# Kernel tuning notes

Measured on AMD Instinct MI355X. Metric: run time of the kernel, lower is better.

## Reference

```python
import jax, jax.numpy as jnp
import numpy as np

EPS = 1e-8  # torch F.cosine_similarity norm clamp


def setup_inputs() -> dict:
    key = jax.random.key(0)
    k1, k2, k3, k4 = jax.random.split(key, 4)
    B, N, M, D, T = 8, 4096, 2048, 512, 2
    return {
        "features": jax.random.normal(k1, (B, N, D), dtype=jnp.float32),
        "text": jax.random.normal(k2, (T, M, D), dtype=jnp.float32),
        "W": jax.random.normal(k3, (D, D), dtype=jnp.float32) * 0.02,
        "b": jax.random.normal(k4, (D,), dtype=jnp.float32) * 0.02,
    }


def reference(features, text, W, b):
    # features: [B, N, D] (output of the extractor), text: [T, M, D]
    B, N, D = features.shape
    f1 = jnp.einsum("bnd,de->bne", features, W) + b  # linear_layer(features)
    t1 = text[1]  # [M, D]; expanded across batch (row 1 per original code)

    # cosine similarity over last dim without materializing [B, N, M, D]
    fn = f1 / jnp.maximum(jnp.linalg.norm(f1, axis=-1, keepdims=True), EPS)
    tn = t1 / jnp.maximum(jnp.linalg.norm(t1, axis=-1, keepdims=True), EPS)
    sim = jnp.einsum("bnd,md->bnm", fn, tn)  # [B, N, M]

    e = jnp.exp(sim)
    w = e / jnp.sum(e, axis=1, keepdims=True)  # normalize over N (dim=1)

    # features_t [B,D,N] @ w [B,N,M] -> [B,D,M] -> transpose -> [B,M,D]
    fm = jnp.einsum("bnd,bnm->bmd", features, w)

    t1b = jnp.broadcast_to(t1[None, :, :], (B,) + t1.shape)  # [B, M, D]
    combine_feature = jnp.concatenate([fm, t1b], axis=2)  # [B, M, 2D]
    return combine_feature
```

## Files before the change

kernel.cpp:

```cpp
#include <hip/hip_runtime.h>

#define B_SZ 8
#define N_SZ 4096
#define M_SZ 2048
#define D_SZ 512

typedef __attribute__((ext_vector_type(8))) short bf16x8;
typedef __attribute__((ext_vector_type(4))) float f32x4;
typedef __attribute__((address_space(1))) const void* gptr1;
typedef __attribute__((address_space(3))) void* lptr3;

__device__ __forceinline__ unsigned short f2bf(float x) {
    unsigned int u = __builtin_bit_cast(unsigned int, x);
    u += 0x7fffu + ((u >> 16) & 1u);
    return (unsigned short)(u >> 16);
}

__device__ __forceinline__ void bt_mainloop(
    const unsigned short* __restrict__ A, const unsigned short* __restrict__ Bt,
    int lda, int ldb, int rowBase, int colBase, int K,
    unsigned short* As, unsigned short* Bs, f32x4 acc[4][4])
{
    const int tid  = threadIdx.x;
    const int lane = tid & 63;
    const int w    = tid >> 6;
    const int wr   = (w >> 1) * 64;
    const int wc   = (w & 1) * 64;
    const int lr   = lane & 15;
    const int kq   = lane >> 4;

    const int srow0 = w * 16 + (lane >> 2);
    const int skk   = (lane & 3) * 8;

    for (int k0 = 0; k0 < K; k0 += 32) {
#pragma unroll
        for (int j = 0; j < 2; ++j) {
            const unsigned short* ga = A  + (size_t)(rowBase + srow0 + j * 64) * lda + (k0 + skk);
            const unsigned short* gb = Bt + (size_t)(colBase + srow0 + j * 64) * ldb + (k0 + skk);
            __builtin_amdgcn_global_load_lds((gptr1)ga, (lptr3)(As + (j * 4 + w) * 512), 16, 0, 0);
            __builtin_amdgcn_global_load_lds((gptr1)gb, (lptr3)(Bs + (j * 4 + w) * 512), 16, 0, 0);
        }
        asm volatile("s_waitcnt vmcnt(0)" ::: "memory");
        __syncthreads();

        bf16x8 af[4], bq[4];
#pragma unroll
        for (int i = 0; i < 4; ++i) {
            af[i] = *(const bf16x8*)(As + (wr + i * 16 + lr) * 32 + kq * 8);
            bq[i] = *(const bf16x8*)(Bs + (wc + i * 16 + lr) * 32 + kq * 8);
        }
#pragma unroll
        for (int mi = 0; mi < 4; ++mi)
#pragma unroll
            for (int ni = 0; ni < 4; ++ni)
                acc[mi][ni] = __builtin_amdgcn_mfma_f32_16x16x32_bf16(af[mi], bq[ni], acc[mi][ni], 0, 0, 0);
        __syncthreads();
    }
}

#define GEMM_PROLOGUE() \
    __shared__ unsigned short As[128 * 32]; \
    __shared__ unsigned short Bs[128 * 32]; \
    f32x4 acc[4][4]; \
    _Pragma("unroll") for (int i = 0; i < 4; ++i) \
        _Pragma("unroll") for (int j = 0; j < 4; ++j) \
            acc[i][j] = (f32x4){0.f, 0.f, 0.f, 0.f}; \
    const int tid = threadIdx.x; const int lane = tid & 63; const int w = tid >> 6; \
    const int wr = (w >> 1) * 64, wc = (w & 1) * 64, lr = lane & 15, kq = lane >> 4; \
    (void)tid;

__global__ __launch_bounds__(256) void prep_tn_k(
    const float* __restrict__ text, unsigned short* __restrict__ tn,
    float* __restrict__ out, float* __restrict__ L)
{
    const int m = blockIdx.x;
    const int t = threadIdx.x;
    const float* t1 = text + (size_t)M_SZ * D_SZ;
    float2 v = ((const float2*)(t1 + (size_t)m * D_SZ))[t];
    float s = v.x * v.x + v.y * v.y;
#pragma unroll
    for (int off = 32; off > 0; off >>= 1) s += __shfl_down(s, off);
    __shared__ float partial[4];
    if ((t & 63) == 0) partial[t >> 6] = s;
    __syncthreads();
    float norm = sqrtf(partial[0] + partial[1] + partial[2] + partial[3]);
    norm = fmaxf(norm, 1e-8f);
    const float inv = 1.f / norm;
    ushort2 pk; pk.x = f2bf(v.x * inv); pk.y = f2bf(v.y * inv);
    ((ushort2*)(tn + (size_t)m * D_SZ))[t] = pk;
#pragma unroll
    for (int b = 0; b < B_SZ; ++b)
        ((float2*)(out + ((size_t)(b * M_SZ + m)) * (2 * D_SZ) + D_SZ))[t] = v;
    if (m < 64) L[m * 256 + t] = 0.f;
}

__global__ __launch_bounds__(256) void prep_w_k(
    const float* __restrict__ W, unsigned short* __restrict__ Wt)
{
    const int dt = blockIdx.x, et = blockIdx.y;
    const int t = threadIdx.x;
    __shared__ unsigned short tile[64][72];
    const int rr = t >> 4;
    const int cc = (t & 15) * 4;
#pragma unroll
    for (int p = 0; p < 4; ++p) {
        const int d = p * 16 + rr;
        const float4 v = *(const float4*)(W + (size_t)(dt * 64 + d) * D_SZ + et * 64 + cc);
        tile[d][cc] = f2bf(v.x); tile[d][cc + 1] = f2bf(v.y);
        tile[d][cc + 2] = f2bf(v.z); tile[d][cc + 3] = f2bf(v.w);
    }
    __syncthreads();
#pragma unroll
    for (int p = 0; p < 4; ++p) {
        const int e = p * 16 + rr;
        ushort4 pk;
        pk.x = tile[cc][e]; pk.y = tile[cc + 1][e]; pk.z = tile[cc + 2][e]; pk.w = tile[cc + 3][e];
        *(ushort4*)(Wt + (size_t)(et * 64 + e) * D_SZ + dt * 64 + cc) = pk;
    }
}

__global__ __launch_bounds__(256) void convert_feat_k(
    const float* __restrict__ feat, unsigned short* __restrict__ V,
    unsigned short* __restrict__ Vt)
{
    const int nt = blockIdx.x, dt = blockIdx.y, b = blockIdx.z;
    const int t = threadIdx.x;
    __shared__ unsigned short tile[64][72];
    const int rr = t >> 4;
    const int cc = (t & 15) * 4;
#pragma unroll
    for (int p = 0; p < 4; ++p) {
        const int r = p * 16 + rr;
        const size_t grow = (size_t)(b * N_SZ + nt * 64 + r);
        const float4 v = *(const float4*)(feat + grow * D_SZ + dt * 64 + cc);
        ushort4 pk; pk.x = f2bf(v.x); pk.y = f2bf(v.y); pk.z = f2bf(v.z); pk.w = f2bf(v.w);
        *(ushort4*)(V + grow * D_SZ + dt * 64 + cc) = pk;
        tile[r][cc] = pk.x; tile[r][cc + 1] = pk.y; tile[r][cc + 2] = pk.z; tile[r][cc + 3] = pk.w;
    }
    __syncthreads();
#pragma unroll
    for (int p = 0; p < 4; ++p) {
        const int d = p * 16 + rr;
        ushort4 pk;
        pk.x = tile[cc][d]; pk.y = tile[cc + 1][d]; pk.z = tile[cc + 2][d]; pk.w = tile[cc + 3][d];
        *(ushort4*)(Vt + ((size_t)(b * D_SZ + dt * 64 + d)) * N_SZ + nt * 64 + cc) = pk;
    }
}

__global__ __launch_bounds__(256) void gemm1_k(
    const unsigned short* __restrict__ V, const unsigned short* __restrict__ Wt,
    const float* __restrict__ bias, float* __restrict__ f1)
{
    GEMM_PROLOGUE();
    const int rowBase = blockIdx.x * 128;
    const int colBase = blockIdx.y * 128;
    bt_mainloop(V, Wt, D_SZ, D_SZ, rowBase, colBase, D_SZ, As, Bs, acc);
#pragma unroll
    for (int mi = 0; mi < 4; ++mi) {
        const int r0 = rowBase + wr + mi * 16 + kq * 4;
#pragma unroll
        for (int ni = 0; ni < 4; ++ni) {
            const int c = colBase + wc + ni * 16 + lr;
            const float bv = bias[c];
#pragma unroll
            for (int r = 0; r < 4; ++r)
                f1[(size_t)(r0 + r) * D_SZ + c] = acc[mi][ni][r] + bv;
        }
    }
}

__global__ __launch_bounds__(128) void normalize_k(
    const float* __restrict__ f1, unsigned short* __restrict__ fn)
{
    const int row = blockIdx.x;
    const int t = threadIdx.x;
    const float4 v = ((const float4*)(f1 + (size_t)row * D_SZ))[t];
    float s = v.x * v.x + v.y * v.y + v.z * v.z + v.w * v.w;
#pragma unroll
    for (int off = 32; off > 0; off >>= 1) s += __shfl_down(s, off);
    __shared__ float partial[2];
    if ((t & 63) == 0) partial[t >> 6] = s;
    __syncthreads();
    float norm = sqrtf(partial[0] + partial[1]);
    norm = fmaxf(norm, 1e-8f);
    const float inv = 1.f / norm;
    ushort4 pk;
    pk.x = f2bf(v.x * inv); pk.y = f2bf(v.y * inv);
    pk.z = f2bf(v.z * inv); pk.w = f2bf(v.w * inv);
    ((ushort4*)(fn + (size_t)row * D_SZ))[t] = pk;
}

__global__ __launch_bounds__(256) void gemm2_k(
    const unsigned short* __restrict__ fn, const unsigned short* __restrict__ tn,
    unsigned short* __restrict__ E, float* __restrict__ L)
{
    GEMM_PROLOGUE();
    const int rowBase = blockIdx.x * 128;
    const int colBase = blockIdx.y * 128;
    bt_mainloop(fn, tn, D_SZ, D_SZ, rowBase, colBase, D_SZ, As, Bs, acc);

    const int b  = rowBase >> 12;
    const int nb = rowBase & 4095;
    unsigned short* Eb = E + (size_t)b * M_SZ * N_SZ;
#pragma unroll
    for (int ni = 0; ni < 4; ++ni) {
        const int m = colBase + wc + ni * 16 + lr;
        float p = 0.f;
#pragma unroll
        for (int mi = 0; mi < 4; ++mi) {
            const int n0 = nb + wr + mi * 16 + kq * 4;
            const float e0 = __expf(acc[mi][ni][0]);
            const float e1 = __expf(acc[mi][ni][1]);
            const float e2 = __expf(acc[mi][ni][2]);
            const float e3 = __expf(acc[mi][ni][3]);
            ushort4 pk; pk.x = f2bf(e0); pk.y = f2bf(e1); pk.z = f2bf(e2); pk.w = f2bf(e3);
            *(ushort4*)(Eb + (size_t)m * N_SZ + n0) = pk;
            p += (e0 + e1) + (e2 + e3);
        }
        p += __shfl_down(p, 16);
        p += __shfl_down(p, 32);
        if (lane < 16) atomicAdd(&L[b * M_SZ + m], p);
    }
}

__global__ __launch_bounds__(256) void gemm3_k(
    const unsigned short* __restrict__ E, const unsigned short* __restrict__ Vt,
    const float* __restrict__ L, float* __restrict__ out)
{
    GEMM_PROLOGUE();
    const int b = blockIdx.z;
    const int rowBase = blockIdx.x * 128;
    const int colBase = blockIdx.y * 128;
    const unsigned short* Ab = E + (size_t)b * M_SZ * N_SZ;
    const unsigned short* Bb = Vt + (size_t)b * D_SZ * N_SZ;
    bt_mainloop(Ab, Bb, N_SZ, N_SZ, rowBase, colBase, N_SZ, As, Bs, acc);

#pragma unroll
    for (int mi = 0; mi < 4; ++mi) {
        const int r0 = rowBase + wr + mi * 16 + kq * 4;
        float invl[4];
#pragma unroll
        for (int r = 0; r < 4; ++r) invl[r] = 1.f / L[b * M_SZ + r0 + r];
#pragma unroll
        for (int ni = 0; ni < 4; ++ni) {
            const int d = colBase + wc + ni * 16 + lr;
#pragma unroll
            for (int r = 0; r < 4; ++r)
                out[((size_t)(b * M_SZ + r0 + r)) * (2 * D_SZ) + d] = acc[mi][ni][r] * invl[r];
        }
    }
}

extern "C" void kernel_launch(void* const* d_in, const int* in_sizes, int n_in,
                              void* d_out, int out_size, void* d_ws, size_t ws_size,
                              hipStream_t stream) {
    const float* features = (const float*)d_in[0];
    const float* text     = (const float*)d_in[1];
    const float* W        = (const float*)d_in[2];
    const float* bias     = (const float*)d_in[3];
    float* out = (float*)d_out;
    char* ws = (char*)d_ws;

    unsigned short* fn = (unsigned short*)(ws + 0);
    unsigned short* tn = (unsigned short*)(ws + 33554432);
    unsigned short* Wt = (unsigned short*)(ws + 35651584);
    unsigned short* V  = (unsigned short*)(ws + 36175872);
    unsigned short* Vt = (unsigned short*)(ws + 69730304);
    float*          L  = (float*)(ws + 103284736);
    float*          f1 = (float*)(ws + 103350272);
    unsigned short* E  = (unsigned short*)(ws + 103350272);

    hipLaunchKernelGGL(prep_tn_k, dim3(M_SZ), dim3(256), 0, stream, text, tn, out, L);
    hipLaunchKernelGGL(prep_w_k, dim3(8, 8), dim3(256), 0, stream, W, Wt);
    hipLaunchKernelGGL(convert_feat_k, dim3(64, 8, 8), dim3(256), 0, stream, features, V, Vt);
    hipLaunchKernelGGL(gemm1_k, dim3(256, 4), dim3(256), 0, stream, V, Wt, bias, f1);
    hipLaunchKernelGGL(normalize_k, dim3(32768), dim3(128), 0, stream, f1, fn);
    hipLaunchKernelGGL(gemm2_k, dim3(256, 16), dim3(256), 0, stream, fn, tn, E, L);
    hipLaunchKernelGGL(gemm3_k, dim3(16, 4, 8), dim3(256), 0, stream, E, Vt, L, out);
}
```

Baseline: 408.6 us.

## Fuse row sum-of-squares into gemm1, store bf16, and coalesce gemm2 stores via LDS

gemm1 now writes its output in bf16 and accumulates per-row sums of squares with atomics, so normalize_k reads half the bytes and skips its block reduction. gemm2 stages the exp tile in LDS and writes E with wide coalesced row stores instead of scattered 8-byte writes. It also remaps block indices so row tiles are spread across XCDs, which may improve L2 locality. The cost is an extra bf16 rounding before normalization and atomics on the sum-of-squares buffer.

```diff
diff --git a/kernel.cpp b/kernel.cpp
--- a/kernel.cpp
+++ b/kernel.cpp
@@ -14,6 +14,10 @@
     unsigned int u = __builtin_bit_cast(unsigned int, x);
     u += 0x7fffu + ((u >> 16) & 1u);
     return (unsigned short)(u >> 16);
+}
+__device__ __forceinline__ float bf2f(unsigned short u) {
+    unsigned int x = ((unsigned int)u) << 16;
+    return __builtin_bit_cast(float, x);
 }
 
 __device__ __forceinline__ void bt_mainloop(
@@ -58,20 +62,9 @@
     }
 }
 
-#define GEMM_PROLOGUE() \
-    __shared__ unsigned short As[128 * 32]; \
-    __shared__ unsigned short Bs[128 * 32]; \
-    f32x4 acc[4][4]; \
-    _Pragma("unroll") for (int i = 0; i < 4; ++i) \
-        _Pragma("unroll") for (int j = 0; j < 4; ++j) \
-            acc[i][j] = (f32x4){0.f, 0.f, 0.f, 0.f}; \
-    const int tid = threadIdx.x; const int lane = tid & 63; const int w = tid >> 6; \
-    const int wr = (w >> 1) * 64, wc = (w & 1) * 64, lr = lane & 15, kq = lane >> 4; \
-    (void)tid;
-
 __global__ __launch_bounds__(256) void prep_tn_k(
     const float* __restrict__ text, unsigned short* __restrict__ tn,
-    float* __restrict__ out, float* __restrict__ L)
+    float* __restrict__ out, float* __restrict__ L, float* __restrict__ SS)
 {
     const int m = blockIdx.x;
     const int t = threadIdx.x;
@@ -92,6 +85,7 @@
     for (int b = 0; b < B_SZ; ++b)
         ((float2*)(out + ((size_t)(b * M_SZ + m)) * (2 * D_SZ) + D_SZ))[t] = v;
     if (m < 64) L[m * 256 + t] = 0.f;
+    if (m < 128) SS[m * 256 + t] = 0.f;
 }
 
 __global__ __launch_bounds__(256) void prep_w_k(
@@ -149,77 +143,121 @@
 
 __global__ __launch_bounds__(256) void gemm1_k(
     const unsigned short* __restrict__ V, const unsigned short* __restrict__ Wt,
-    const float* __restrict__ bias, float* __restrict__ f1)
-{
-    GEMM_PROLOGUE();
+    const float* __restrict__ bias, unsigned short* __restrict__ f1b,
+    float* __restrict__ SS)
+{
+    __shared__ unsigned short As[128 * 32];
+    __shared__ unsigned short Bs[128 * 32];
+    f32x4 acc[4][4];
+#pragma unroll
+    for (int i = 0; i < 4; ++i)
+#pragma unroll
+        for (int j = 0; j < 4; ++j) acc[i][j] = (f32x4){0.f, 0.f, 0.f, 0.f};
+    const int tid = threadIdx.x, lane = tid & 63, w = tid >> 6;
+    const int wr = (w >> 1) * 64, wc = (w & 1) * 64, lr = lane & 15, kq = lane >> 4;
+
     const int rowBase = blockIdx.x * 128;
     const int colBase = blockIdx.y * 128;
     bt_mainloop(V, Wt, D_SZ, D_SZ, rowBase, colBase, D_SZ, As, Bs, acc);
+
 #pragma unroll
     for (int mi = 0; mi < 4; ++mi) {
         const int r0 = rowBase + wr + mi * 16 + kq * 4;
+        float s[4] = {0.f, 0.f, 0.f, 0.f};
 #pragma unroll
         for (int ni = 0; ni < 4; ++ni) {
             const int c = colBase + wc + ni * 16 + lr;
             const float bv = bias[c];
 #pragma unroll
-            for (int r = 0; r < 4; ++r)
-                f1[(size_t)(r0 + r) * D_SZ + c] = acc[mi][ni][r] + bv;
+            for (int r = 0; r < 4; ++r) {
+                const float v = acc[mi][ni][r] + bv;
+                f1b[(size_t)(r0 + r) * D_SZ + c] = f2bf(v);
+                s[r] += v * v;
+            }
+        }
+#pragma unroll
+        for (int off = 1; off <= 8; off <<= 1)
+#pragma unroll
+            for (int r = 0; r < 4; ++r) s[r] += __shfl_xor(s[r], off);
+        if (lr == 0) {
+#pragma unroll
+            for (int r = 0; r < 4; ++r) atomicAdd(&SS[r0 + r], s[r]);
         }
     }
 }
 
 __global__ __launch_bounds__(128) void normalize_k(
-    const float* __restrict__ f1, unsigned short* __restrict__ fn)
+    const unsigned short* __restrict__ f1b, const float* __restrict__ SS,
+    unsigned short* __restrict__ fn)
 {
     const int row = blockIdx.x;
     const int t = threadIdx.x;
-    const float4 v = ((const float4*)(f1 + (size_t)row * D_SZ))[t];
-    float s = v.x * v.x + v.y * v.y + v.z * v.z + v.w * v.w;
-#pragma unroll
-    for (int off = 32; off > 0; off >>= 1) s += __shfl_down(s, off);
-    __shared__ float partial[2];
-    if ((t & 63) == 0) partial[t >> 6] = s;
-    __syncthreads();
-    float norm = sqrtf(partial[0] + partial[1]);
-    norm = fmaxf(norm, 1e-8f);
+    const float norm = fmaxf(sqrtf(SS[row]), 1e-8f);
     const float inv = 1.f / norm;
-    ushort4 pk;
-    pk.x = f2bf(v.x * inv); pk.y = f2bf(v.y * inv);
-    pk.z = f2bf(v.z * inv); pk.w = f2bf(v.w * inv);
-    ((ushort4*)(fn + (size_t)row * D_SZ))[t] = pk;
+    ushort4 v = ((const ushort4*)(f1b + (size_t)row * D_SZ))[t];
+    ushort4 o;
+    o.x = f2bf(bf2f(v.x) * inv); o.y = f2bf(bf2f(v.y) * inv);
+    o.z = f2bf(bf2f(v.z) * inv); o.w = f2bf(bf2f(v.w) * inv);
+    ((ushort4*)(fn + (size_t)row * D_SZ))[t] = o;
 }
 
 __global__ __launch_bounds__(256) void gemm2_k(
     const unsigned short* __restrict__ fn, const unsigned short* __restrict__ tn,
     unsigned short* __restrict__ E, float* __restrict__ L)
 {
-    GEMM_PROLOGUE();
-    const int rowBase = blockIdx.x * 128;
-    const int colBase = blockIdx.y * 128;
+    __shared__ unsigned short smem[128 * 136];
+    unsigned short* As = smem;
+    unsigned short* Bs = smem + 4096;
+    f32x4 acc[4][4];
+#pragma unroll
+    for (int i = 0; i < 4; ++i)
+#pragma unroll
+        for (int j = 0; j < 4; ++j) acc[i][j] = (f32x4){0.f, 0.f, 0.f, 0.f};
+    const int tid = threadIdx.x, lane = tid & 63, w = tid >> 6;
+    const int wr = (w >> 1) * 64, wc = (w & 1) * 64, lr = lane & 15, kq = lane >> 4;
+
+    const int lin = blockIdx.x;
+    const int xcd = lin & 7, slot = lin >> 3;
+    const int mt = slot & 15;
+    const int rt = (slot >> 4) * 8 + xcd;
+    const int rowBase = rt * 128;
+    const int colBase = mt * 128;
+
     bt_mainloop(fn, tn, D_SZ, D_SZ, rowBase, colBase, D_SZ, As, Bs, acc);
 
     const int b  = rowBase >> 12;
     const int nb = rowBase & 4095;
     unsigned short* Eb = E + (size_t)b * M_SZ * N_SZ;
+    unsigned short* P = smem;
+
 #pragma unroll
     for (int ni = 0; ni < 4; ++ni) {
-        const int m = colBase + wc + ni * 16 + lr;
+        const int mm = wc + ni * 16 + lr;
         float p = 0.f;
 #pragma unroll
         for (int mi = 0; mi < 4; ++mi) {
-            const int n0 = nb + wr + mi * 16 + kq * 4;
+            const int nn0 = wr + mi * 16 + kq * 4;
             const float e0 = __expf(acc[mi][ni][0]);
             const float e1 = __expf(acc[mi][ni][1]);
             const float e2 = __expf(acc[mi][ni][2]);
             const float e3 = __expf(acc[mi][ni][3]);
             ushort4 pk; pk.x = f2bf(e0); pk.y = f2bf(e1); pk.z = f2bf(e2); pk.w = f2bf(e3);
-            *(ushort4*)(Eb + (size_t)m * N_SZ + n0) = pk;
+            *(ushort4*)(P + mm * 136 + nn0) = pk;
             p += (e0 + e1) + (e2 + e3);
         }
         p += __shfl_down(p, 16);
         p += __shfl_down(p, 32);
-        if (lane < 16) atomicAdd(&L[b * M_SZ + m], p);
+        if (lane < 16) atomicAdd(&L[b * M_SZ + colBase + mm], p);
+    }
+    __syncthreads();
+
+    const int tr = tid >> 4;
+    const int tc = (tid & 15) * 8;
+#pragma unroll
+    for (int j = 0; j < 8; ++j) {
+        const int mm = j * 16 + tr;
+        bf16x8 v = *(const bf16x8*)(P + mm * 136 + tc);
+        *(bf16x8*)(Eb + (size_t)(colBase + mm) * N_SZ + nb + tc) = v;
     }
 }
 
@@ -227,7 +265,16 @@
     const unsigned short* __restrict__ E, const unsigned short* __restrict__ Vt,
     const float* __restrict__ L, float* __restrict__ out)
 {
-    GEMM_PROLOGUE();
+    __shared__ unsigned short As[128 * 32];
+    __shared__ unsigned short Bs[128 * 32];
+    f32x4 acc[4][4];
+#pragma unroll
+    for (int i = 0; i < 4; ++i)
+#pragma unroll
+        for (int j = 0; j < 4; ++j) acc[i][j] = (f32x4){0.f, 0.f, 0.f, 0.f};
+    const int tid = threadIdx.x, lane = tid & 63, w = tid >> 6;
+    const int wr = (w >> 1) * 64, wc = (w & 1) * 64, lr = lane & 15, kq = lane >> 4;
+
     const int b = blockIdx.z;
     const int rowBase = blockIdx.x * 128;
     const int colBase = blockIdx.y * 128;
@@ -261,20 +308,21 @@
     float* out = (float*)d_out;
     char* ws = (char*)d_ws;
 
-    unsigned short* fn = (unsigned short*)(ws + 0);
-    unsigned short* tn = (unsigned short*)(ws + 33554432);
-    unsigned short* Wt = (unsigned short*)(ws + 35651584);
-    unsigned short* V  = (unsigned short*)(ws + 36175872);
-    unsigned short* Vt = (unsigned short*)(ws + 69730304);
-    float*          L  = (float*)(ws + 103284736);
-    float*          f1 = (float*)(ws + 103350272);
-    unsigned short* E  = (unsigned short*)(ws + 103350272);
-
-    hipLaunchKernelGGL(prep_tn_k, dim3(M_SZ), dim3(256), 0, stream, text, tn, out, L);
+    unsigned short* fn  = (unsigned short*)(ws + 0);
+    unsigned short* tn  = (unsigned short*)(ws + 33554432);
+    unsigned short* Wt  = (unsigned short*)(ws + 35651584);
+    unsigned short* V   = (unsigned short*)(ws + 36175872);
+    unsigned short* Vt  = (unsigned short*)(ws + 69730304);
+    float*          L   = (float*)(ws + 103284736);
+    float*          SS  = (float*)(ws + 103350272);
+    unsigned short* E   = (unsigned short*)(ws + 103481344);
+    unsigned short* f1b = (unsigned short*)(ws + 103481344);
+
+    hipLaunchKernelGGL(prep_tn_k, dim3(M_SZ), dim3(256), 0, stream, text, tn, out, L, SS);
     hipLaunchKernelGGL(prep_w_k, dim3(8, 8), dim3(256), 0, stream, W, Wt);
     hipLaunchKernelGGL(convert_feat_k, dim3(64, 8, 8), dim3(256), 0, stream, features, V, Vt);
-    hipLaunchKernelGGL(gemm1_k, dim3(256, 4), dim3(256), 0, stream, V, Wt, bias, f1);
-    hipLaunchKernelGGL(normalize_k, dim3(32768), dim3(128), 0, stream, f1, fn);
-    hipLaunchKernelGGL(gemm2_k, dim3(256, 16), dim3(256), 0, stream, fn, tn, E, L);
+    hipLaunchKernelGGL(gemm1_k, dim3(256, 4), dim3(256), 0, stream, V, Wt, bias, f1b, SS);
+    hipLaunchKernelGGL(normalize_k, dim3(32768), dim3(128), 0, stream, f1b, SS, fn);
+    hipLaunchKernelGGL(gemm2_k, dim3(4096), dim3(256), 0, stream, fn, tn, E, L);
     hipLaunchKernelGGL(gemm3_k, dim3(16, 4, 8), dim3(256), 0, stream, E, Vt, L, out);
 }
```

Result: faster. 383.5 us (-6.2%).
